# Optimization experiments

Measured on AMD Instinct MI355X. Metric: run time of the kernel, lower is better.

## Reference

```python
import jax, jax.numpy as jnp
import numpy as np
import math

STAGE_NUM = 5
EPS = 1e-6

def _l2norm(a, axis):
    return a / (EPS + jnp.linalg.norm(a, axis=axis, keepdims=True))

def setup_inputs() -> dict:
    key = jax.random.key(0)
    k1, k2, k3, k4 = jax.random.split(key, 4)
    b, n, c, h, w, k, out_c = 4, 4, 256, 64, 64, 128, 256
    x = jax.random.normal(k1, (b, c, h, w), dtype=jnp.float32)
    querys = jax.random.normal(k2, (b * n, c, h, w), dtype=jnp.float32)
    # mu init: normal(0, sqrt(2/k)) then l2norm over channel dim
    mu0 = jax.random.normal(k3, (1, c, k), dtype=jnp.float32) * math.sqrt(2.0 / k)
    mu0 = _l2norm(mu0, axis=1)
    # conv weight: normal(0, sqrt(2/(kh*kw*out_c)))
    fan = 3 * 3 * out_c
    conv_w = jax.random.normal(k4, (out_c, 2 * c, 3, 3), dtype=jnp.float32) * math.sqrt(2.0 / fan)
    conv_b = jnp.zeros((out_c,), dtype=jnp.float32)
    return {"x": x, "querys": querys, "mu0": mu0, "conv_w": conv_w, "conv_b": conv_b, "n": n}

def reference(x, querys, mu0, conv_w, conv_b, n):
    b, c, h, w = x.shape
    k = mu0.shape[2]
    xf = x.reshape(b, c, h * w)                       # [b, c, L]
    mu = jnp.broadcast_to(mu0, (b, c, k))

    # EM iterations (torch.no_grad -> stop_gradient)
    def em_step(mu, _):
        z = jnp.einsum('bcl,bck->blk', xf, mu)        # [b, L, k]
        z = jax.nn.softmax(z, axis=2)
        z_ = z / (EPS + jnp.sum(z, axis=1, keepdims=True))
        mu = jnp.einsum('bcl,blk->bck', xf, z_)       # [b, c, k]
        mu = _l2norm(mu, axis=1)
        return mu, None
    mu, _ = jax.lax.scan(em_step, mu, None, length=STAGE_NUM)
    mu = jax.lax.stop_gradient(mu)

    org_query = querys                                 # [b*n, c, h, w]
    q = querys.reshape(b, n, c, h, w).transpose(0, 2, 1, 3, 4).reshape(b, c, n * h * w)
    q_z = jax.nn.softmax(jnp.einsum('bcl,bck->blk', q, mu), axis=2)  # [b, nL, k]
    q_z = jax.lax.stop_gradient(q_z)

    rec = jnp.einsum('bck,blk->bcl', mu, q_z)          # [b, c, n*h*w]
    rec = rec.reshape(b, c, n, h, w).transpose(0, 2, 1, 3, 4).reshape(b * n, c, h, w)

    cat = jnp.concatenate((org_query, rec), axis=1)    # [b*n, 2c, h, w]
    out = jax.lax.conv_general_dilated(
        cat, conv_w, window_strides=(1, 1), padding='SAME',
        dimension_numbers=('NCHW', 'OIHW', 'NCHW'))
    out = out + conv_b[None, :, None, None]
    return (out, mu)
```

## Files before the change

### kernel.cpp

```cpp
#include <hip/hip_runtime.h>
#include <hip/hip_bf16.h>

#define B   4
#define NN  4
#define C   256
#define HH  64
#define WW  64
#define L   4096
#define NL  16384
#define K   128
#define OC  256
#define IC2 512
#define EPSV 1e-6f
#define PW  66
#define PA  4356

typedef __hip_bfloat16 bf16;
typedef __attribute__((ext_vector_type(8))) __bf16 bf16x8;
typedef __attribute__((ext_vector_type(4))) float f32x4;

#define AS1(p) ((const __attribute__((address_space(1))) void*)(p))
#define AS3(p) ((__attribute__((address_space(3))) void*)(p))

__global__ void k_init(const float* __restrict__ mu0, float* __restrict__ mu_f,
                       bf16* __restrict__ mub) {
    int i = blockIdx.x * 256 + threadIdx.x;
    int rem = i & 32767;
    int k = rem >> 8, c = rem & 255;
    float v = mu0[c * 128 + k];
    mu_f[i] = v;
    mub[i]  = __float2bfloat16(v);
}

__global__ void k_prepx(const float* __restrict__ x, bf16* __restrict__ xb,
                        bf16* __restrict__ xt) {
    __shared__ float ld[64][65];
    int lt = blockIdx.x, ct = blockIdx.y, b = blockIdx.z;
    int t = threadIdx.x;
    #pragma unroll
    for (int i = 0; i < 16; i++) {
        int idx = t + i * 256;
        int ch = idx >> 6, xl = idx & 63;
        size_t a = ((size_t)b * C + ct * 64 + ch) * L + lt * 64 + xl;
        float v = x[a];
        ld[ch][xl] = v;
        xb[a] = __float2bfloat16(v);
    }
    __syncthreads();
    #pragma unroll
    for (int i = 0; i < 16; i++) {
        int idx = t + i * 256;
        int xl = idx >> 6, ch = idx & 63;
        xt[((size_t)b * L + lt * 64 + xl) * 256 + ct * 64 + ch] = __float2bfloat16(ld[ch][xl]);
    }
}

__global__ void k_prepq(const float* __restrict__ qy, bf16* __restrict__ P2) {
    __shared__ float ld[64][65];
    int y = blockIdx.x, ct = blockIdx.y, img = blockIdx.z;
    int t = threadIdx.x;
    #pragma unroll
    for (int i = 0; i < 16; i++) {
        int idx = t + i * 256;
        int ch = idx >> 6, xl = idx & 63;
        ld[ch][xl] = qy[((size_t)img * C + ct * 64 + ch) * L + y * WW + xl];
    }
    __syncthreads();
    #pragma unroll
    for (int i = 0; i < 16; i++) {
        int idx = t + i * 256;
        int xl = idx >> 6, ch = idx & 63;
        P2[((size_t)img * PA + (size_t)(y + 1) * PW + xl + 1) * 512 + ct * 64 + ch] =
            __float2bfloat16(ld[ch][xl]);
    }
}

__global__ void k_zborder(uint4* __restrict__ P2) {
    int pi = blockIdx.x, img = blockIdx.y, t = threadIdx.x;
    int y, x;
    if      (pi < 66)  { y = 0;        x = pi; }
    else if (pi < 132) { y = 65;       x = pi - 66; }
    else if (pi < 196) { y = pi - 131; x = 0; }
    else               { y = pi - 195; x = 65; }
    P2[((size_t)img * PA + (size_t)y * PW + x) * 64 + t] = uint4{0, 0, 0, 0};
}

__global__ void k_wprep(const float* __restrict__ cw, bf16* __restrict__ wb) {
    int idx = blockIdx.x * 256 + threadIdx.x;
    if (idx >= 9 * OC * IC2) return;
    int r  = idx / (OC * IC2);
    int oc = (idx / IC2) & 255;
    int ic = idx & 511;
    wb[idx] = __float2bfloat16(cw[((size_t)oc * IC2 + ic) * 9 + r]);
}

__global__ void __launch_bounds__(256) k_z(const bf16* __restrict__ xt,
                                           const bf16* __restrict__ mub,
                                           bf16* __restrict__ zt) {
    __shared__ __align__(16) char smem[12288];
    char* tA = smem;
    char* tB = smem + 8192;
    int t = threadIdx.x, w = t >> 6, lane = t & 63;
    int b = blockIdx.y, l0 = blockIdx.x * 64;
    const bf16* Ab = mub + (size_t)b * K * C;
    const bf16* Bb = xt + ((size_t)b * L + l0) * C;
    int srow = t >> 2, sseg = t & 3, aseg = sseg ^ (srow & 3);
    char* dA0 = tA + w * 1024;
    char* dA1 = tA + 4096 + w * 1024;
    char* dB  = tB + w * 1024;
    int aoff[8], boff;
    #pragma unroll
    for (int i = 0; i < 8; i++) {
        int rowA = i * 16 + (lane & 15);
        aoff[i] = rowA * 64 + (((lane >> 4) ^ (rowA & 3)) << 4);
    }
    { int rowB = w * 16 + (lane & 15);
      boff = rowB * 64 + (((lane >> 4) ^ (rowB & 3)) << 4); }
    f32x4 acc[8];
    #pragma unroll
    for (int i = 0; i < 8; i++) acc[i] = f32x4{0.f, 0.f, 0.f, 0.f};
    for (int s = 0; s < 8; s++) {
        int cb0 = s * 32 + aseg * 8;
        __syncthreads();
        __builtin_amdgcn_global_load_lds(AS1(Ab + (size_t)srow * C + cb0),        AS3(dA0), 16, 0, 0);
        __builtin_amdgcn_global_load_lds(AS1(Ab + (size_t)(srow + 64) * C + cb0), AS3(dA1), 16, 0, 0);
        __builtin_amdgcn_global_load_lds(AS1(Bb + (size_t)srow * C + cb0),        AS3(dB),  16, 0, 0);
        __syncthreads();
        bf16x8 bfr = *(bf16x8*)(tB + boff);
        #pragma unroll
        for (int i = 0; i < 8; i++) {
            bf16x8 af = *(bf16x8*)(tA + aoff[i]);
            acc[i] = __builtin_amdgcn_mfma_f32_16x16x32_bf16(af, bfr, acc[i], 0, 0, 0);
        }
    }
    float m = -1e30f;
    #pragma unroll
    for (int i = 0; i < 8; i++)
        #pragma unroll
        for (int r = 0; r < 4; r++) m = fmaxf(m, acc[i][r]);
    m = fmaxf(m, __shfl_xor(m, 16, 64));
    m = fmaxf(m, __shfl_xor(m, 32, 64));
    float ssum = 0.f;
    #pragma unroll
    for (int i = 0; i < 8; i++)
        #pragma unroll
        for (int r = 0; r < 4; r++) { acc[i][r] = __expf(acc[i][r] - m); ssum += acc[i][r]; }
    ssum += __shfl_xor(ssum, 16, 64);
    ssum += __shfl_xor(ssum, 32, 64);
    float inv = 1.f / ssum;
    int quad = lane >> 4, col = lane & 15;
    bf16* zb = zt + (size_t)b * K * L + l0 + w * 16 + col;
    #pragma unroll
    for (int i = 0; i < 8; i++)
        #pragma unroll
        for (int r = 0; r < 4; r++) {
            int k = i * 16 + quad * 4 + r;
            zb[(size_t)k * L] = __float2bfloat16(acc[i][r] * inv);
        }
}

__global__ void __launch_bounds__(256) k_mu(const bf16* __restrict__ zt,
                                            const bf16* __restrict__ xb,
                                            float* __restrict__ part) {
    __shared__ __align__(16) char smem[16384];
    char* tA = smem; char* tB = smem + 8192;
    int t = threadIdx.x, w = t >> 6, lane = t & 63;
    int ct = blockIdx.x, chunk = blockIdx.y, b = blockIdx.z;
    const bf16* Ab = zt + (size_t)b * K * L + chunk * 256;
    const bf16* Bb = xb + ((size_t)b * C + ct * 128) * L + chunk * 256;
    int srow = t >> 2, sseg = t & 3, aseg = sseg ^ (srow & 3);
    char* dA0 = tA + w * 1024; char* dA1 = tA + 4096 + w * 1024;
    char* dB0 = tB + w * 1024; char* dB1 = tB + 4096 + w * 1024;
    int wm = w >> 1, wn = w & 1;
    int aoff[4], boff[4];
    #pragma unroll
    for (int i = 0; i < 4; i++) {
        int rowA = wm * 64 + i * 16 + (lane & 15);
        aoff[i] = rowA * 64 + (((lane >> 4) ^ (rowA & 3)) << 4);
        int rowB = wn * 64 + i * 16 + (lane & 15);
        boff[i] = rowB * 64 + (((lane >> 4) ^ (rowB & 3)) << 4);
    }
    f32x4 acc[4][4];
    #pragma unroll
    for (int i = 0; i < 4; i++)
        #pragma unroll
        for (int j = 0; j < 4; j++) acc[i][j] = f32x4{0.f, 0.f, 0.f, 0.f};
    for (int s = 0; s < 8; s++) {
        int lb = s * 32 + aseg * 8;
        __syncthreads();
        __builtin_amdgcn_global_load_lds(AS1(Ab + (size_t)srow * L + lb),        AS3(dA0), 16, 0, 0);
        __builtin_amdgcn_global_load_lds(AS1(Ab + (size_t)(srow + 64) * L + lb), AS3(dA1), 16, 0, 0);
        __builtin_amdgcn_global_load_lds(AS1(Bb + (size_t)srow * L + lb),        AS3(dB0), 16, 0, 0);
        __builtin_amdgcn_global_load_lds(AS1(Bb + (size_t)(srow + 64) * L + lb), AS3(dB1), 16, 0, 0);
        __syncthreads();
        bf16x8 af[4], bfr[4];
        #pragma unroll
        for (int i = 0; i < 4; i++) af[i]  = *(bf16x8*)(tA + aoff[i]);
        #pragma unroll
        for (int j = 0; j < 4; j++) bfr[j] = *(bf16x8*)(tB + boff[j]);
        #pragma unroll
        for (int i = 0; i < 4; i++)
            #pragma unroll
            for (int j = 0; j < 4; j++)
                acc[i][j] = __builtin_amdgcn_mfma_f32_16x16x32_bf16(af[i], bfr[j], acc[i][j], 0, 0, 0);
    }
    float* pb = part + ((size_t)(b * 16 + chunk) * K) * C + ct * 128;
    int quad = lane >> 4, col = lane & 15;
    #pragma unroll
    for (int i = 0; i < 4; i++) {
        int k = wm * 64 + i * 16 + quad * 4;
        #pragma unroll
        for (int j = 0; j < 4; j++) {
            int c = wn * 64 + j * 16 + col;
            #pragma unroll
            for (int r = 0; r < 4; r++)
                pb[(size_t)(k + r) * C + c] = acc[i][j][r];
        }
    }
}

__global__ void k_norm(const float* __restrict__ part, float* __restrict__ mu_f,
                       bf16* __restrict__ mub, bf16* __restrict__ muT) {
    int b = blockIdx.x >> 7, k = blockIdx.x & 127, lane = threadIdx.x;
    float v[4] = {0.f, 0.f, 0.f, 0.f};
    for (int ch = 0; ch < 16; ch++) {
        const float* p = part + ((size_t)(b * 16 + ch) * K + k) * C;
        #pragma unroll
        for (int j = 0; j < 4; j++) v[j] += p[lane + j * 64];
    }
    float s = v[0]*v[0] + v[1]*v[1] + v[2]*v[2] + v[3]*v[3];
    for (int o = 32; o > 0; o >>= 1) s += __shfl_xor(s, o, 64);
    float r = 1.f / (EPSV + sqrtf(s));
    float* mf = mu_f + ((size_t)b * K + k) * C;
    bf16*  mb = mub  + ((size_t)b * K + k) * C;
    bf16*  mt = muT  + (size_t)b * C * K + k;
    #pragma unroll
    for (int j = 0; j < 4; j++) {
        float val = v[j] * r;
        int c = lane + j * 64;
        mf[c] = val;
        mb[c] = __float2bfloat16(val);
        mt[(size_t)c * K] = __float2bfloat16(val);
    }
}

__global__ void __launch_bounds__(256) k_qz(const bf16* __restrict__ P2,
                                            const bf16* __restrict__ mub,
                                            bf16* __restrict__ qz) {
    __shared__ __align__(16) char smem[12288];
    char* tA = smem;
    char* tB = smem + 4096;
    int t = threadIdx.x, w = t >> 6, lane = t & 63;
    int b = blockIdx.y, tile = blockIdx.x;
    int n = tile >> 6, y = tile & 63;
    int img = b * NN + n;
    const bf16* Ab = P2 + ((size_t)img * PA + (size_t)(y + 1) * PW + 1) * 512;
    const bf16* Bb = mub + (size_t)b * K * C;
    int srow = t >> 2, sseg = t & 3, aseg = sseg ^ (srow & 3);
    char* dA  = tA + w * 1024;
    char* dB0 = tB + w * 1024;
    char* dB1 = tB + 4096 + w * 1024;
    int boff[8], aoff;
    #pragma unroll
    for (int j = 0; j < 8; j++) {
        int rowB = j * 16 + (lane & 15);
        boff[j] = rowB * 64 + (((lane >> 4) ^ (rowB & 3)) << 4);
    }
    { int rowA = w * 16 + (lane & 15);
      aoff = rowA * 64 + (((lane >> 4) ^ (rowA & 3)) << 4); }
    f32x4 acc[8];
    #pragma unroll
    for (int j = 0; j < 8; j++) acc[j] = f32x4{0.f, 0.f, 0.f, 0.f};
    for (int s = 0; s < 8; s++) {
        int cb0 = s * 32 + aseg * 8;
        __syncthreads();
        __builtin_amdgcn_global_load_lds(AS1(Ab + (size_t)srow * 512 + cb0),      AS3(dA),  16, 0, 0);
        __builtin_amdgcn_global_load_lds(AS1(Bb + (size_t)srow * C + cb0),        AS3(dB0), 16, 0, 0);
        __builtin_amdgcn_global_load_lds(AS1(Bb + (size_t)(srow + 64) * C + cb0), AS3(dB1), 16, 0, 0);
        __syncthreads();
        bf16x8 af = *(bf16x8*)(tA + aoff);
        #pragma unroll
        for (int j = 0; j < 8; j++) {
            bf16x8 bfr = *(bf16x8*)(tB + boff[j]);
            acc[j] = __builtin_amdgcn_mfma_f32_16x16x32_bf16(af, bfr, acc[j], 0, 0, 0);
        }
    }
    int quad = lane >> 4, col = lane & 15;
    bf16* qb = qz + ((size_t)b * NL + n * L + y * WW + w * 16 + quad * 4) * K;
    #pragma unroll
    for (int r = 0; r < 4; r++) {
        float mm = acc[0][r];
        #pragma unroll
        for (int j = 1; j < 8; j++) mm = fmaxf(mm, acc[j][r]);
        mm = fmaxf(mm, __shfl_xor(mm, 1, 64));
        mm = fmaxf(mm, __shfl_xor(mm, 2, 64));
        mm = fmaxf(mm, __shfl_xor(mm, 4, 64));
        mm = fmaxf(mm, __shfl_xor(mm, 8, 64));
        float ss = 0.f;
        float e[8];
        #pragma unroll
        for (int j = 0; j < 8; j++) { e[j] = __expf(acc[j][r] - mm); ss += e[j]; }
        ss += __shfl_xor(ss, 1, 64);
        ss += __shfl_xor(ss, 2, 64);
        ss += __shfl_xor(ss, 4, 64);
        ss += __shfl_xor(ss, 8, 64);
        float inv = 1.f / ss;
        #pragma unroll
        for (int j = 0; j < 8; j++)
            qb[(size_t)r * K + j * 16 + col] = __float2bfloat16(e[j] * inv);
    }
}

__global__ void __launch_bounds__(256) k_rec(const bf16* __restrict__ qz,
                                             const bf16* __restrict__ muT,
                                             bf16* __restrict__ P2) {
    __shared__ __align__(16) char smem[16384];
    char* tA = smem; char* tB = smem + 8192;
    int t = threadIdx.x, w = t >> 6, lane = t & 63;
    int ct = blockIdx.x, lt = blockIdx.y, b = blockIdx.z;
    const bf16* Ab = qz + ((size_t)b * NL + lt * 128) * K;
    const bf16* Bb = muT + ((size_t)b * C + ct * 128) * K;
    int srow = t >> 2, sseg = t & 3, aseg = sseg ^ (srow & 3);
    char* dA0 = tA + w * 1024; char* dA1 = tA + 4096 + w * 1024;
    char* dB0 = tB + w * 1024; char* dB1 = tB + 4096 + w * 1024;
    int wm = w >> 1, wn = w & 1;
    int aoff[4], boff[4];
    #pragma unroll
    for (int i = 0; i < 4; i++) {
        int rowA = wm * 64 + i * 16 + (lane & 15);
        aoff[i] = rowA * 64 + (((lane >> 4) ^ (rowA & 3)) << 4);
        int rowB = wn * 64 + i * 16 + (lane & 15);
        boff[i] = rowB * 64 + (((lane >> 4) ^ (rowB & 3)) << 4);
    }
    f32x4 acc[4][4];
    #pragma unroll
    for (int i = 0; i < 4; i++)
        #pragma unroll
        for (int j = 0; j < 4; j++) acc[i][j] = f32x4{0.f, 0.f, 0.f, 0.f};
    for (int s = 0; s < 4; s++) {
        int kb = s * 32 + aseg * 8;
        __syncthreads();
        __builtin_amdgcn_global_load_lds(AS1(Ab + (size_t)srow * K + kb),        AS3(dA0), 16, 0, 0);
        __builtin_amdgcn_global_load_lds(AS1(Ab + (size_t)(srow + 64) * K + kb), AS3(dA1), 16, 0, 0);
        __builtin_amdgcn_global_load_lds(AS1(Bb + (size_t)srow * K + kb),        AS3(dB0), 16, 0, 0);
        __builtin_amdgcn_global_load_lds(AS1(Bb + (size_t)(srow + 64) * K + kb), AS3(dB1), 16, 0, 0);
        __syncthreads();
        bf16x8 af[4], bfr[4];
        #pragma unroll
        for (int i = 0; i < 4; i++) af[i]  = *(bf16x8*)(tA + aoff[i]);
        #pragma unroll
        for (int j = 0; j < 4; j++) bfr[j] = *(bf16x8*)(tB + boff[j]);
        #pragma unroll
        for (int i = 0; i < 4; i++)
            #pragma unroll
            for (int j = 0; j < 4; j++)
                acc[i][j] = __builtin_amdgcn_mfma_f32_16x16x32_bf16(af[i], bfr[j], acc[i][j], 0, 0, 0);
    }
    int quad = lane >> 4, col = lane & 15;
    #pragma unroll
    for (int i = 0; i < 4; i++) {
        int lbase = lt * 128 + wm * 64 + i * 16 + quad * 4;
        #pragma unroll
        for (int r = 0; r < 4; r++) {
            int l = lbase + r;
            int n = l >> 12, p = l & 4095;
            int y = p >> 6, xp = p & 63;
            bf16* dst = P2 + ((size_t)(b * NN + n) * PA + (size_t)(y + 1) * PW + xp + 1) * 512 + 256;
            #pragma unroll
            for (int j = 0; j < 4; j++)
                dst[ct * 128 + wn * 64 + j * 16 + col] = __float2bfloat16(acc[i][j][r]);
        }
    }
}

__global__ void __launch_bounds__(256, 2) k_conv(const bf16* __restrict__ P2,
                                                 const bf16* __restrict__ Wb,
                                                 const float* __restrict__ cb,
                                                 float* __restrict__ out) {
    __shared__ __align__(16) char smem[49920];
    char* inl = smem;
    char* wld = smem + 25344;
    int t = threadIdx.x, w = t >> 6, lane = t & 63;
    int m0  = blockIdx.x * 128;
    int y0  = blockIdx.y * 4;
    int img = blockIdx.z;
    int srow = t >> 2;
    int aseg = (t & 3) ^ ((srow ^ (srow >> 2)) & 3);
    int wm = w >> 1, wn = w & 1;
    int q = lane >> 4, lane15 = lane & 15;

    int aoff[4];
    #pragma unroll
    for (int i = 0; i < 4; i++) {
        int rowA = wm * 64 + i * 16 + lane15;
        aoff[i] = rowA * 64 + (((q ^ (rowA ^ (rowA >> 2))) & 3) << 4);
    }

    auto stageIN = [&](int cc) {
        size_t ibase = (size_t)img * PA * 512 + cc * 32;
        #pragma unroll
        for (int it = 0; it < 6; it++) {
            unsigned g = it * 256 + t;
            unsigned row = g / 264u, ps = g - row * 264u;
            unsigned px = ps >> 2, s0 = ps & 3;
            unsigned sg = s0 ^ ((px ^ (px >> 1)) & 3);
            __builtin_amdgcn_global_load_lds(
                AS1(P2 + ibase + ((size_t)(y0 + row) * PW + px) * 512 + sg * 8),
                AS3(inl + it * 4096 + w * 1024), 16, 0, 0);
        }
        if (t < 48) {
            unsigned g = 1536 + t;
            unsigned row = g / 264u, ps = g - row * 264u;
            unsigned px = ps >> 2, s0 = ps & 3;
            unsigned sg = s0 ^ ((px ^ (px >> 1)) & 3);
            __builtin_amdgcn_global_load_lds(
                AS1(P2 + ibase + ((size_t)(y0 + row) * PW + px) * 512 + sg * 8),
                AS3(inl + 24576), 16, 0, 0);
        }
    };

    f32x4 acc[4][8];
    #pragma unroll
    for (int i = 0; i < 4; i++) {
        int oc = m0 + wm * 64 + i * 16 + q * 4;
        #pragma unroll
        for (int r = 0; r < 4; r++) {
            float bv = cb[oc + r];
            #pragma unroll
            for (int j = 0; j < 8; j++) acc[i][j][r] = bv;
        }
    }

    stageIN(0);
    {
        const bf16* w0 = Wb + (size_t)(m0 + srow) * IC2 + aseg * 8;
        __builtin_amdgcn_global_load_lds(AS1(w0),                         AS3(wld + w * 1024), 16, 0, 0);
        __builtin_amdgcn_global_load_lds(AS1(w0 + (size_t)64 * IC2),      AS3(wld + 4096 + w * 1024), 16, 0, 0);
        const bf16* w1 = w0 + (size_t)(OC * IC2);
        __builtin_amdgcn_global_load_lds(AS1(w1),                         AS3(wld + 8192 + w * 1024), 16, 0, 0);
        __builtin_amdgcn_global_load_lds(AS1(w1 + (size_t)64 * IC2),      AS3(wld + 8192 + 4096 + w * 1024), 16, 0, 0);
    }
    asm volatile("s_waitcnt vmcnt(0)" ::: "memory");
    __builtin_amdgcn_s_barrier();
    asm volatile("" ::: "memory");

    for (int cc = 0; cc < 16; cc++) {
        #pragma unroll
        for (int rt = 0; rt < 9; rt++) {
            const int dy = rt / 3, dx = rt % 3;
            char* wbuf = wld + (rt % 3) * 8192;
            bf16x8 af[4];
            #pragma unroll
            for (int i = 0; i < 4; i++) af[i] = *(bf16x8*)(wbuf + aoff[i]);
            const bool doPf = (cc * 9 + rt + 2) < 144;
            if (doPf) {
                const int g2 = rt + 2;
                const int rt2 = (g2 >= 9) ? g2 - 9 : g2;
                const int cc2 = cc + (g2 >= 9 ? 1 : 0);
                char* wdst = wld + ((rt + 2) % 3) * 8192;
                const bf16* wsrc = Wb + (size_t)rt2 * (OC * IC2) + (size_t)(m0 + srow) * IC2
                                 + cc2 * 32 + aseg * 8;
                __builtin_amdgcn_global_load_lds(AS1(wsrc),                    AS3(wdst + w * 1024), 16, 0, 0);
                __builtin_amdgcn_global_load_lds(AS1(wsrc + (size_t)64 * IC2), AS3(wdst + 4096 + w * 1024), 16, 0, 0);
            }
            __builtin_amdgcn_s_setprio(1);
            #pragma unroll
            for (int j = 0; j < 8; j++) {
                int p = (j & 3) * 16 + lane15 + dx;
                int rowsel = 2 * wn + (j >> 2) + dy;
                bf16x8 bfr = *(bf16x8*)(inl + rowsel * 4224 + p * 64 +
                                        (((q ^ (p ^ (p >> 1))) & 3) << 4));
                #pragma unroll
                for (int i = 0; i < 4; i++)
                    acc[i][j] = __builtin_amdgcn_mfma_f32_16x16x32_bf16(af[i], bfr, acc[i][j], 0, 0, 0);
            }
            __builtin_amdgcn_s_setprio(0);
            if (rt == 8) {
                if (cc < 15) {
                    asm volatile("" ::: "memory");
                    __builtin_amdgcn_s_barrier();
                    asm volatile("" ::: "memory");
                    stageIN(cc + 1);
                    asm volatile("s_waitcnt vmcnt(0)" ::: "memory");
                    __builtin_amdgcn_s_barrier();
                    asm volatile("" ::: "memory");
                }
            } else {
                if (doPf) asm volatile("s_waitcnt vmcnt(2)" ::: "memory");
                else      asm volatile("s_waitcnt vmcnt(0)" ::: "memory");
                __builtin_amdgcn_s_barrier();
                asm volatile("" ::: "memory");
            }
        }
    }

    #pragma unroll
    for (int i = 0; i < 4; i++) {
        int oc = m0 + wm * 64 + i * 16 + q * 4;
        #pragma unroll
        for (int j = 0; j < 8; j++) {
            int px = blockIdx.y * 256 + wn * 128 + (j >> 2) * 64 + (j & 3) * 16 + lane15;
            #pragma unroll
            for (int r = 0; r < 4; r++)
                out[((size_t)img * OC + oc + r) * L + px] = acc[i][j][r];
        }
    }
}

__global__ void k_muout(const float* __restrict__ mu_f, float* __restrict__ out) {
    int i = blockIdx.x * 256 + threadIdx.x;
    int b = i >> 15, rem = i & 32767;
    int c = rem >> 7, k = rem & 127;
    out[(size_t)16777216 + i] = mu_f[((size_t)b * K + k) * C + c];
}

extern "C" void kernel_launch(void* const* d_in, const int* in_sizes, int n_in,
                              void* d_out, int out_size, void* d_ws, size_t ws_size,
                              hipStream_t stream) {
    const float* x   = (const float*)d_in[0];
    const float* qy  = (const float*)d_in[1];
    const float* mu0 = (const float*)d_in[2];
    const float* cw  = (const float*)d_in[3];
    const float* cb  = (const float*)d_in[4];
    float* out = (float*)d_out;

    char* ws = (char*)d_ws;
    float* mu_f = (float*)(ws);
    bf16*  mu_b = (bf16*) (ws + 524288);
    bf16*  muT  = (bf16*) (ws + 786432);
    bf16*  Wb   = (bf16*) (ws + 1048576);
    bf16*  zt   = (bf16*) (ws + 3407872);
    bf16*  qz   = (bf16*) (ws + 3407872);
    bf16*  P2   = (bf16*) (ws + 20185088);
    bf16*  x_bf = (bf16*) (ws + 20185088);
    float* part = (float*)(ws + 20185088 + 8388608);
    bf16*  xt   = (bf16*) (ws + 20185088 + 16777216);

    k_init<<<512, 256, 0, stream>>>(mu0, mu_f, mu_b);
    k_prepx<<<dim3(64, 4, 4), 256, 0, stream>>>(x, x_bf, xt);

    for (int it = 0; it < 5; it++) {
        k_z<<<dim3(64, 4), 256, 0, stream>>>(xt, mu_b, zt);
        k_mu<<<dim3(2, 16, 4), 256, 0, stream>>>(zt, x_bf, part);
        k_norm<<<512, 64, 0, stream>>>(part, mu_f, mu_b, muT);
    }

    k_prepq<<<dim3(64, 4, 16), 256, 0, stream>>>(qy, P2);
    k_zborder<<<dim3(260, 16), 64, 0, stream>>>((uint4*)P2);
    k_wprep<<<4608, 256, 0, stream>>>(cw, Wb);

    k_qz<<<dim3(256, 4), 256, 0, stream>>>(P2, mu_b, qz);
    k_rec<<<dim3(2, 128, 4), 256, 0, stream>>>(qz, muT, P2);
    k_conv<<<dim3(2, 16, 16), 256, 0, stream>>>(P2, Wb, cb, out);
    k_muout<<<512, 256, 0, stream>>>(mu_f, out);
}
```

Measured before the change: 410.9 us.

## Double-buffer conv input tile and spread its prefetch across filter taps

The conv kernel now keeps two LDS buffers for the padded input tile. The next channel chunk's input is loaded in seven slices interleaved with the first seven filter taps of the current chunk, instead of being staged all at once behind a full barrier and a vmcnt(0) drain at each chunk boundary. This is meant to hide input-load latency behind MFMA work and remove one barrier per chunk. LDS use grows from about 49KB to 75KB per block, which may cut occupancy under the launch bound of 2 blocks per CU, and the hand-tuned vmcnt counts must match the number of outstanding loads exactly.

```diff
diff --git a/kernel.cpp b/kernel.cpp
--- a/kernel.cpp
+++ b/kernel.cpp
@@ -377,9 +377,9 @@
                                                  const bf16* __restrict__ Wb,
                                                  const float* __restrict__ cb,
                                                  float* __restrict__ out) {
-    __shared__ __align__(16) char smem[49920];
+    __shared__ __align__(16) char smem[75264];
     char* inl = smem;
-    char* wld = smem + 25344;
+    char* wld = smem + 50688;
     int t = threadIdx.x, w = t >> 6, lane = t & 63;
     int m0  = blockIdx.x * 128;
     int y0  = blockIdx.y * 4;
@@ -396,26 +396,16 @@
         aoff[i] = rowA * 64 + (((q ^ (rowA ^ (rowA >> 2))) & 3) << 4);
     }
 
-    auto stageIN = [&](int cc) {
-        size_t ibase = (size_t)img * PA * 512 + cc * 32;
-        #pragma unroll
-        for (int it = 0; it < 6; it++) {
-            unsigned g = it * 256 + t;
-            unsigned row = g / 264u, ps = g - row * 264u;
-            unsigned px = ps >> 2, s0 = ps & 3;
-            unsigned sg = s0 ^ ((px ^ (px >> 1)) & 3);
+    size_t inbase = (size_t)img * PA * 512;
+    auto stagePart = [&](int cc, int s, int buf) {
+        if (s < 6 || lane < 12) {
+            unsigned e = w * 396u + s * 64u + (unsigned)lane;
+            unsigned row = e / 264u, ps = e - row * 264u;
+            unsigned px = ps >> 2;
+            unsigned sg = (ps & 3) ^ ((px ^ (px >> 1)) & 3);
             __builtin_amdgcn_global_load_lds(
-                AS1(P2 + ibase + ((size_t)(y0 + row) * PW + px) * 512 + sg * 8),
-                AS3(inl + it * 4096 + w * 1024), 16, 0, 0);
-        }
-        if (t < 48) {
-            unsigned g = 1536 + t;
-            unsigned row = g / 264u, ps = g - row * 264u;
-            unsigned px = ps >> 2, s0 = ps & 3;
-            unsigned sg = s0 ^ ((px ^ (px >> 1)) & 3);
-            __builtin_amdgcn_global_load_lds(
-                AS1(P2 + ibase + ((size_t)(y0 + row) * PW + px) * 512 + sg * 8),
-                AS3(inl + 24576), 16, 0, 0);
+                AS1(P2 + inbase + ((size_t)(y0 + row) * PW + px) * 512 + cc * 32 + sg * 8),
+                AS3(inl + buf * 25344 + w * 6336 + s * 1024), 16, 0, 0);
         }
     };
 
@@ -431,19 +421,21 @@
         }
     }
 
-    stageIN(0);
+    #pragma unroll
+    for (int s = 0; s < 7; s++) stagePart(0, s, 0);
     {
         const bf16* w0 = Wb + (size_t)(m0 + srow) * IC2 + aseg * 8;
-        __builtin_amdgcn_global_load_lds(AS1(w0),                         AS3(wld + w * 1024), 16, 0, 0);
-        __builtin_amdgcn_global_load_lds(AS1(w0 + (size_t)64 * IC2),      AS3(wld + 4096 + w * 1024), 16, 0, 0);
+        __builtin_amdgcn_global_load_lds(AS1(w0),                    AS3(wld + w * 1024), 16, 0, 0);
+        __builtin_amdgcn_global_load_lds(AS1(w0 + (size_t)64 * IC2), AS3(wld + 4096 + w * 1024), 16, 0, 0);
         const bf16* w1 = w0 + (size_t)(OC * IC2);
-        __builtin_amdgcn_global_load_lds(AS1(w1),                         AS3(wld + 8192 + w * 1024), 16, 0, 0);
-        __builtin_amdgcn_global_load_lds(AS1(w1 + (size_t)64 * IC2),      AS3(wld + 8192 + 4096 + w * 1024), 16, 0, 0);
-    }
-    asm volatile("s_waitcnt vmcnt(0)" ::: "memory");
+        __builtin_amdgcn_global_load_lds(AS1(w1),                    AS3(wld + 8192 + w * 1024), 16, 0, 0);
+        __builtin_amdgcn_global_load_lds(AS1(w1 + (size_t)64 * IC2), AS3(wld + 8192 + 4096 + w * 1024), 16, 0, 0);
+    }
+    asm volatile("s_waitcnt vmcnt(2)" ::: "memory");
     __builtin_amdgcn_s_barrier();
     asm volatile("" ::: "memory");
 
+    int inb = 0;
     for (int cc = 0; cc < 16; cc++) {
         #pragma unroll
         for (int rt = 0; rt < 9; rt++) {
@@ -452,6 +444,7 @@
             bf16x8 af[4];
             #pragma unroll
             for (int i = 0; i < 4; i++) af[i] = *(bf16x8*)(wbuf + aoff[i]);
+            if (cc < 15 && rt < 7) stagePart(cc + 1, rt, inb ^ 1);
             const bool doPf = (cc * 9 + rt + 2) < 144;
             if (doPf) {
                 const int g2 = rt + 2;
@@ -468,7 +461,7 @@
             for (int j = 0; j < 8; j++) {
                 int p = (j & 3) * 16 + lane15 + dx;
                 int rowsel = 2 * wn + (j >> 2) + dy;
-                bf16x8 bfr = *(bf16x8*)(inl + rowsel * 4224 + p * 64 +
+                bf16x8 bfr = *(bf16x8*)(inl + inb * 25344 + rowsel * 4224 + p * 64 +
                                         (((q ^ (p ^ (p >> 1))) & 3) << 4));
                 #pragma unroll
                 for (int i = 0; i < 4; i++)
@@ -477,17 +470,19 @@
             __builtin_amdgcn_s_setprio(0);
             if (rt == 8) {
                 if (cc < 15) {
-                    asm volatile("" ::: "memory");
+                    asm volatile("s_waitcnt vmcnt(2)" ::: "memory");
                     __builtin_amdgcn_s_barrier();
                     asm volatile("" ::: "memory");
-                    stageIN(cc + 1);
-                    asm volatile("s_waitcnt vmcnt(0)" ::: "memory");
-                    __builtin_amdgcn_s_barrier();
-                    asm volatile("" ::: "memory");
+                    inb ^= 1;
                 }
+            } else if (cc < 15) {
+                if (rt < 7) asm volatile("s_waitcnt vmcnt(3)" ::: "memory");
+                else        asm volatile("s_waitcnt vmcnt(2)" ::: "memory");
+                __builtin_amdgcn_s_barrier();
+                asm volatile("" ::: "memory");
             } else {
-                if (doPf) asm volatile("s_waitcnt vmcnt(2)" ::: "memory");
-                else      asm volatile("s_waitcnt vmcnt(0)" ::: "memory");
+                if (rt < 7) asm volatile("s_waitcnt vmcnt(2)" ::: "memory");
+                else        asm volatile("s_waitcnt vmcnt(0)" ::: "memory");
                 __builtin_amdgcn_s_barrier();
                 asm volatile("" ::: "memory");
             }
```

New measurement: 454.4 us. 1.11x slower.
